# Optimization experiments

Hardware: AMD Instinct MI355X
Metric: run time of the kernel (lower is better)

## Reference

```python
import jax, jax.numpy as jnp
import numpy as np

B, GH, GW, NUM_HEADS, DIM = 8, 32, 32, 16, 1024
HEAD_DIM = DIM // NUM_HEADS  # 64
N = GH * GW  # 1024


def _rope_cos_sin(head_dim, h, w):
    # Lumina-style 2D rotary embedding: head_dim/2 complex rotations,
    # interleaving H-axis and W-axis frequencies: [h0, w0, h1, w1, ...].
    nf = head_dim // 4  # freqs per axis
    theta = 1.0 / (10000.0 ** (np.arange(0, head_dim // 2, 2, dtype=np.float32) / (head_dim // 2)))
    ang_h = np.arange(h, dtype=np.float32)[:, None] * theta[None, :]  # (h, nf)
    ang_w = np.arange(w, dtype=np.float32)[:, None] * theta[None, :]  # (w, nf)
    ang = np.zeros((h, w, head_dim // 2), dtype=np.float32)
    ang[..., 0::2] = ang_h[:, None, :]
    ang[..., 1::2] = ang_w[None, :, :]
    ang = ang.reshape(h * w, head_dim // 2)  # (N, d/2)
    return jnp.asarray(np.cos(ang)), jnp.asarray(np.sin(ang))


def _apply_rope(x, cos, sin):
    # x: (B, nh, N, d); pairs (x[2k], x[2k+1]) form complex numbers,
    # rotated by exp(i*ang) per position. cos/sin: (N, d/2).
    xr, xi = x[..., 0::2], x[..., 1::2]
    out_r = xr * cos - xi * sin
    out_i = xr * sin + xi * cos
    return jnp.stack([out_r, out_i], axis=-1).reshape(x.shape)


def setup_inputs() -> dict:
    key = jax.random.key(0)
    k1, k2, k3 = jax.random.split(key, 3)
    return {
        "x": jax.random.normal(k1, (B, N, DIM), dtype=jnp.float32),
        "wqkv_w": jax.random.normal(k2, (3 * DIM, DIM), dtype=jnp.float32) * 0.02,
        "wqkv_b": jnp.zeros((3 * DIM,), dtype=jnp.float32),
        "out_w": jax.random.normal(k3, (DIM, DIM), dtype=jnp.float32) * 0.02,
        "out_b": jnp.zeros((DIM,), dtype=jnp.float32),
    }


def reference(x, wqkv_w, wqkv_b, out_w, out_b):
    Bs, Ns, C = x.shape
    qkv = x @ wqkv_w.T + wqkv_b  # (B, N, 3*C)
    qkv = qkv.reshape(Bs, Ns, 3, NUM_HEADS, HEAD_DIM).transpose(2, 0, 3, 1, 4)
    q, k, v = qkv[0], qkv[1], qkv[2]  # each (B, nh, N, hd)
    cos, sin = _rope_cos_sin(HEAD_DIM, GH, GW)
    q = _apply_rope(q, cos, sin)
    k = _apply_rope(k, cos, sin)
    scale = HEAD_DIM ** -0.5
    attn = jax.nn.softmax((q * scale) @ jnp.swapaxes(k, -1, -2), axis=-1)  # (B, nh, N, N)
    o = attn @ v  # (B, nh, N, hd)
    o = jnp.swapaxes(o, 1, 2).reshape(Bs, Ns, C)
    out = o @ out_w.T + out_b
    return (out,)
```

## Files before the change

### kernel.cpp

```cpp
#include <hip/hip_runtime.h>
#include <math.h>

#define NB   8
#define NSEQ 1024
#define CDIM 1024
#define NH   16
#define HD   64
#define TC   3072

typedef unsigned short u16;
typedef __attribute__((ext_vector_type(8))) _Float16 f16x8;
typedef __attribute__((ext_vector_type(4))) float f32x4;

#define Q_U   ((size_t)0)
#define K_U   ((size_t)8388608)
#define V_U   ((size_t)16777216)
#define XH_U  ((size_t)25165824)
#define WQH_U ((size_t)33554432)
#define OWH_U ((size_t)36700160)
#define CS_B  ((size_t)100663296)

__device__ inline u16 f16b(float f) {
  union { _Float16 h; u16 u; } c;
  c.h = (_Float16)f;
  return c.u;
}
__device__ inline void gload16(const u16* g, u16* l) {
  __builtin_amdgcn_global_load_lds(
      (const __attribute__((address_space(1))) void*)g,
      (__attribute__((address_space(3))) void*)l, 16, 0, 0);
}

__global__ __launch_bounds__(256) void rope_table_k(float2* __restrict__ cs) {
  int idx = blockIdx.x * 256 + threadIdx.x;
  if (idx >= NSEQ * 32) return;
  int n = idx >> 5, p = idx & 31;
  int t = p >> 1;
  int pos = (p & 1) ? (n & 31) : (n >> 5);
  float th = (float)pow(10000.0, -(double)t / 16.0);
  float ang = (float)pos * th;
  cs[idx] = make_float2(cosf(ang), sinf(ang));
}

__global__ __launch_bounds__(256) void cvtall_k(const float* __restrict__ x,
                                                const float* __restrict__ wq,
                                                const float* __restrict__ ow,
                                                u16* __restrict__ xh,
                                                u16* __restrict__ wqh,
                                                u16* __restrict__ owh) {
  int gi = blockIdx.x * 256 + threadIdx.x;
  const float* src;
  u16* dst;
  int i;
  if (gi < 2097152) {
    src = x; dst = xh; i = gi;
  } else if (gi < 2883584) {
    src = wq; dst = wqh; i = gi - 2097152;
  } else {
    src = ow; dst = owh; i = gi - 2883584;
  }
  float4 v = ((const float4*)src)[i];
  ushort4 h;
  h.x = f16b(v.x); h.y = f16b(v.y); h.z = f16b(v.z); h.w = f16b(v.w);
  ((ushort4*)dst)[i] = h;
}

__global__ __launch_bounds__(512, 1) void qkv8_k(
    const u16* __restrict__ A, const u16* __restrict__ B,
    const float* __restrict__ bias, u16* __restrict__ q,
    u16* __restrict__ k, u16* __restrict__ v, const float2* __restrict__ cs) {
  __shared__ __align__(16) u16 SM[65536];
  const int K = 1024;

  const int bid = blockIdx.y * 8 + blockIdx.x;
  const int swz = (bid & 7) * 64 + (bid >> 3);
  const int bx = swz & 7, by = swz >> 3;
  const int m0 = by * 128, c0 = bx * 384;

  const int t = threadIdx.x;
  const int l = t & 63, w = t >> 6;
  const int wr = w >> 2, wcol = w & 3;
  const int lr = l & 15, lg = l >> 4;

  const int sr = t >> 2;
  const int sgb = (t & 3) ^ ((sr >> 1) & 3);
  const u16* agA = A + (size_t)(m0 + sr) * K + sgb * 8;
  const u16* agB = B + (size_t)(c0 + sr) * K + sgb * 8;
  const size_t rstep = (size_t)128 * K;

  f32x4 acc[4][6] = {};

  auto stage = [&](int kt) {
    u16* base = SM + (kt & 3) * 16384;
    const int ko = kt * 32;
    gload16(agA + ko, base + t * 8);
    gload16(agB + ko, base + 4096 + t * 8);
    gload16(agB + rstep + ko, base + 8192 + t * 8);
    gload16(agB + 2 * rstep + ko, base + 12288 + t * 8);
  };
  auto compute = [&](int kt) {
    const u16* bA = SM + (kt & 3) * 16384;
    const u16* bB = bA + 4096;
    f16x8 bf[6], af[4];
#pragma unroll
    for (int ni = 0; ni < 6; ni++) {
      const int R = wcol * 96 + ni * 16 + lr;
      bf[ni] = *(const f16x8*)(bB + R * 32 + ((lg ^ ((R >> 1) & 3)) * 8));
    }
#pragma unroll
    for (int mi = 0; mi < 4; mi++) {
      const int R = wr * 64 + mi * 16 + lr;
      af[mi] = *(const f16x8*)(bA + R * 32 + ((lg ^ ((R >> 1) & 3)) * 8));
    }
    __builtin_amdgcn_s_setprio(1);
#pragma unroll
    for (int mi = 0; mi < 4; mi++)
#pragma unroll
      for (int ni = 0; ni < 6; ni++)
        acc[mi][ni] =
            __builtin_amdgcn_mfma_f32_16x16x32_f16(af[mi], bf[ni], acc[mi][ni], 0, 0, 0);
    __builtin_amdgcn_s_setprio(0);
  };

  stage(0);
  stage(1);
  stage(2);

  for (int kt = 0; kt < 32; ++kt) {
    if (kt < 30)
      asm volatile("s_waitcnt vmcnt(8)" ::: "memory");
    else if (kt == 30)
      asm volatile("s_waitcnt vmcnt(4)" ::: "memory");
    else
      asm volatile("s_waitcnt vmcnt(0)" ::: "memory");
    __builtin_amdgcn_s_barrier();
    if (kt < 29) stage(kt + 3);
    compute(kt);
  }

#pragma unroll
  for (int ni = 0; ni < 6; ni++) {
    const int cd0 = c0 + wcol * 96 + ni * 16;
    const int which = cd0 >> 10;
    u16* dst = which == 0 ? q : (which == 1 ? k : v);
    const int h = (cd0 & 1023) >> 6;
    const int dbase = cd0 & 63;
    if (which < 2) {
#pragma unroll
      for (int mi = 0; mi < 4; mi++) {
        const int rbase = m0 + wr * 64 + mi * 16 + lg * 4;
        const int d = dbase + lr;
        const float bv = bias[cd0 + lr];
#pragma unroll
        for (int r = 0; r < 4; r++) {
          const int m = rbase + r;
          const int b = m >> 10, n = m & 1023;
          float y = acc[mi][ni][r] + bv;
          float yp = __shfl_xor(y, 1, 64);
          float2 csv = cs[n * 32 + (d >> 1)];
          y = (l & 1) ? fmaf(yp, csv.y, y * csv.x)
                      : fmaf(-yp, csv.y, y * csv.x);
          dst[(((size_t)b * NH + h) * NSEQ + n) * HD + d] = f16b(y);
        }
      }
    } else {
#pragma unroll
      for (int mi = 0; mi < 4; mi++) {
        const int rbase = m0 + wr * 64 + mi * 16 + lg * 4;
        const int b = rbase >> 10, n0r = rbase & 1023;
        const int d = dbase + lr;
        const float bv = bias[cd0 + lr];
        ushort4 pk;
        pk.x = f16b(acc[mi][ni][0] + bv);
        pk.y = f16b(acc[mi][ni][1] + bv);
        pk.z = f16b(acc[mi][ni][2] + bv);
        pk.w = f16b(acc[mi][ni][3] + bv);
        *(ushort4*)&dst[(((size_t)b * NH + h) * HD + d) * NSEQ + n0r] = pk;
      }
    }
  }
}

__global__ __launch_bounds__(512, 1) void mgemm_k(
    const u16* __restrict__ A, const u16* __restrict__ B,
    const float* __restrict__ bias, float* __restrict__ outF, int K) {
  __shared__ __align__(16) u16 SM[49152];

  const int bid = blockIdx.y * 4 + blockIdx.x;
  const int swz = (bid & 7) * 32 + (bid >> 3);
  const int bx = swz & 3, by = swz >> 2;
  const int m0 = by * 128, c0 = bx * 256;

  const int t = threadIdx.x;
  const int l = t & 63, w = t >> 6;
  const int wr = w >> 2, wcol = w & 3;
  const int lr = l & 15, lg = l >> 4;

  const int sr = t >> 2;
  const int sgb = (t & 3) ^ ((sr >> 1) & 3);
  const u16* agA = A + (size_t)(m0 + sr) * K + sgb * 8;
  const u16* agB = B + (size_t)(c0 + sr) * K + sgb * 8;
  const size_t rstep = (size_t)128 * K;

  f32x4 acc[4][4] = {};

  auto stage = [&](int kt) {
    u16* base = SM + (kt & 3) * 12288;
    const int ko = kt * 32;
    gload16(agA + ko, base + t * 8);
    gload16(agB + ko, base + 4096 + t * 8);
    gload16(agB + rstep + ko, base + 8192 + t * 8);
  };
  auto compute = [&](int kt) {
    const u16* bA = SM + (kt & 3) * 12288;
    const u16* bB = bA + 4096;
    f16x8 bf[4], af[4];
#pragma unroll
    for (int ni = 0; ni < 4; ni++) {
      const int R = wcol * 64 + ni * 16 + lr;
      bf[ni] = *(const f16x8*)(bB + R * 32 + ((lg ^ ((R >> 1) & 3)) * 8));
    }
#pragma unroll
    for (int mi = 0; mi < 4; mi++) {
      const int R = wr * 64 + mi * 16 + lr;
      af[mi] = *(const f16x8*)(bA + R * 32 + ((lg ^ ((R >> 1) & 3)) * 8));
    }
    __builtin_amdgcn_s_setprio(1);
#pragma unroll
    for (int mi = 0; mi < 4; mi++)
#pragma unroll
      for (int ni = 0; ni < 4; ni++)
        acc[mi][ni] =
            __builtin_amdgcn_mfma_f32_16x16x32_f16(af[mi], bf[ni], acc[mi][ni], 0, 0, 0);
    __builtin_amdgcn_s_setprio(0);
  };

  stage(0);
  stage(1);
  stage(2);

  for (int kt = 0; kt < 32; ++kt) {
    if (kt < 30)
      asm volatile("s_waitcnt vmcnt(6)" ::: "memory");
    else if (kt == 30)
      asm volatile("s_waitcnt vmcnt(3)" ::: "memory");
    else
      asm volatile("s_waitcnt vmcnt(0)" ::: "memory");
    __builtin_amdgcn_s_barrier();
    if (kt < 29) stage(kt + 3);
    compute(kt);
  }

  float* fl = (float*)SM;
#pragma unroll
  for (int mi = 0; mi < 4; mi++) {
    __syncthreads();
#pragma unroll
    for (int ni = 0; ni < 4; ni++)
#pragma unroll
      for (int r = 0; r < 4; r++)
        fl[(wr * 16 + lg * 4 + r) * 260 + wcol * 64 + ni * 16 + lr] =
            acc[mi][ni][r];
    __syncthreads();
#pragma unroll
    for (int p = 0; p < 4; p++) {
      const int sr2 = (t >> 6) + p * 8;
      const int sc = (t & 63) * 4;
      float4 vv = *(float4*)&fl[sr2 * 260 + sc];
      float4 bv = *(const float4*)&bias[c0 + sc];
      vv.x += bv.x; vv.y += bv.y; vv.z += bv.z; vv.w += bv.w;
      const int grow = m0 + (sr2 >> 4) * 64 + mi * 16 + (sr2 & 15);
      *(float4*)&outF[(size_t)grow * CDIM + c0 + sc] = vv;
    }
  }
}

__global__ __launch_bounds__(256) void attn_k(const u16* __restrict__ qg0,
                                              const u16* __restrict__ kg0,
                                              const u16* __restrict__ vtg0,
                                              u16* __restrict__ og) {
  __shared__ __align__(16) u16 Ks[8192];
  __shared__ __align__(16) u16 Vt[8192];
  __shared__ __align__(16) u16 Ps[4][1024];
  const int t = threadIdx.x;
  const int l = t & 63, w = t >> 6;
  const int lr = l & 15, lg = l >> 4;
  const int bh = blockIdx.x;
  const int n0 = blockIdx.y * 64;

  f16x8 qf[2];
  {
    const u16* qp = qg0 + ((size_t)bh * NSEQ + n0 + w * 16 + lr) * HD + lg * 8;
#pragma unroll
    for (int c = 0; c < 2; c++) {
      f16x8 raw = *(const f16x8*)(qp + c * 32);
#pragma unroll
      for (int j = 0; j < 8; j++) raw[j] = raw[j] * (_Float16)0.125f;
      qf[c] = raw;
    }
  }

  const int r0 = t >> 3, b0 = (t & 7) ^ (r0 & 7);
  const int r1 = (256 + t) >> 3, b1 = ((256 + t) & 7) ^ (r1 & 7);
  const u16* kgb = kg0 + (size_t)bh * NSEQ * HD;
  const u16* vgb = vtg0 + (size_t)bh * HD * NSEQ;
  const u16* kga0 = kgb + r0 * 64 + b0 * 8;
  const u16* kga1 = kgb + r1 * 64 + b1 * 8;
  const u16* vga0 = vgb + r0 * 1024 + b0 * 8;
  const u16* vga1 = vgb + r1 * 1024 + b1 * 8;

  float l_run[4] = {0.f, 0.f, 0.f, 0.f};
  f32x4 oa[4] = {};

  auto stage = [&](int kt) {
    u16* kd = Ks + (kt & 1) * 4096;
    u16* vd = Vt + (kt & 1) * 4096;
    gload16(kga0 + kt * 4096, kd + t * 8);
    gload16(kga1 + kt * 4096, kd + 2048 + t * 8);
    gload16(vga0 + kt * 64, vd + t * 8);
    gload16(vga1 + kt * 64, vd + 2048 + t * 8);
  };

  stage(0);
  for (int kt = 0; kt < 16; kt++) {
    asm volatile("s_waitcnt vmcnt(0)" ::: "memory");
    __builtin_amdgcn_s_barrier();
    if (kt < 15) stage(kt + 1);
    const u16* kb = Ks + (kt & 1) * 4096;
    const u16* vb = Vt + (kt & 1) * 4096;

    f32x4 s[4] = {};
#pragma unroll
    for (int c = 0; c < 2; c++) {
#pragma unroll
      for (int ni = 0; ni < 4; ni++) {
        const int kr = ni * 16 + lr;
        f16x8 kf = *(const f16x8*)&kb[kr * 64 + (((c * 4 + lg) ^ (kr & 7)) * 8)];
        s[ni] = __builtin_amdgcn_mfma_f32_16x16x32_f16(qf[c], kf, s[ni], 0, 0, 0);
      }
    }

#pragma unroll
    for (int r = 0; r < 4; r++) {
      float p[4], ps = 0.f;
#pragma unroll
      for (int ni = 0; ni < 4; ni++) {
        p[ni] = __expf(s[ni][r] - 4.0f);
        ps += p[ni];
      }
      l_run[r] += ps;
      const int prow = lg * 4 + r;
      const int sw = prow & 7;
#pragma unroll
      for (int ni = 0; ni < 4; ni++)
        Ps[w][prow * 64 + (((ni * 2 + (lr >> 3)) ^ sw) * 8) + (lr & 7)] =
            f16b(p[ni]);
    }

#pragma unroll
    for (int c = 0; c < 2; c++) {
      f16x8 pa = *(const f16x8*)&Ps[w][lr * 64 + (((c * 4 + lg) ^ (lr & 7)) * 8)];
#pragma unroll
      for (int ni = 0; ni < 4; ni++) {
        const int dr = ni * 16 + lr;
        f16x8 vf = *(const f16x8*)&vb[dr * 64 + (((c * 4 + lg) ^ (dr & 7)) * 8)];
        oa[ni] = __builtin_amdgcn_mfma_f32_16x16x32_f16(pa, vf, oa[ni], 0, 0, 0);
      }
    }
  }

  const int b = bh >> 4, h = bh & 15;
#pragma unroll
  for (int r = 0; r < 4; r++) {
    float lv = l_run[r];
    lv += __shfl_xor(lv, 1, 64);
    lv += __shfl_xor(lv, 2, 64);
    lv += __shfl_xor(lv, 4, 64);
    lv += __shfl_xor(lv, 8, 64);
    const float inv = 1.0f / lv;
    const size_t n = n0 + w * 16 + lg * 4 + r;
    const size_t base = ((size_t)b * NSEQ + n) * CDIM + h * HD;
#pragma unroll
    for (int ni = 0; ni < 4; ni++)
      og[base + ni * 16 + lr] = f16b(oa[ni][r] * inv);
  }
}

extern "C" void kernel_launch(void* const* d_in, const int* in_sizes, int n_in,
                              void* d_out, int out_size, void* d_ws, size_t ws_size,
                              hipStream_t stream) {
  const float* x      = (const float*)d_in[0];
  const float* wqkv_w = (const float*)d_in[1];
  const float* wqkv_b = (const float*)d_in[2];
  const float* out_w  = (const float*)d_in[3];
  const float* out_b  = (const float*)d_in[4];
  float* out = (float*)d_out;
  u16* ws = (u16*)d_ws;
  float2* cs = (float2*)((char*)d_ws + CS_B);

  rope_table_k<<<dim3((NSEQ * 32 + 255) / 256), 256, 0, stream>>>(cs);
  cvtall_k<<<dim3(12288), 256, 0, stream>>>(
      x, wqkv_w, out_w, ws + XH_U, ws + WQH_U, ws + OWH_U);

  qkv8_k<<<dim3(8, 64), 512, 0, stream>>>(
      ws + XH_U, ws + WQH_U, wqkv_b, ws + Q_U, ws + K_U, ws + V_U, cs);

  attn_k<<<dim3(NB * NH, NSEQ / 64), 256, 0, stream>>>(
      ws + Q_U, ws + K_U, ws + V_U, ws + XH_U);

  mgemm_k<<<dim3(4, 64), 512, 0, stream>>>(
      ws + XH_U, ws + OWH_U, out_b, out, CDIM);
}
```

Before: 202.1 us.

## Replace LDS-pipelined GEMMs with direct global-to-register MFMA loads

Both the QKV projection and output projection GEMMs drop the multi-stage LDS staging pipeline (async global-to-LDS loads, vmcnt waits, barriers) and instead load MFMA fragments directly from global memory into registers each k-step. The QKV kernel also changes its tile from 128x384 to 256x256 with 8x4 accumulators per wave and a 12x32 grid, simplifying the epilogue to one head per wave. This removes barrier and LDS traffic but loses cross-wave data sharing through LDS, relying on L1/L2 for reuse, and exposes global latency without explicit prefetch.

```diff
diff --git a/kernel.cpp b/kernel.cpp
--- a/kernel.cpp
+++ b/kernel.cpp
@@ -69,88 +69,55 @@
     const u16* __restrict__ A, const u16* __restrict__ B,
     const float* __restrict__ bias, u16* __restrict__ q,
     u16* __restrict__ k, u16* __restrict__ v, const float2* __restrict__ cs) {
-  __shared__ __align__(16) u16 SM[65536];
   const int K = 1024;
 
-  const int bid = blockIdx.y * 8 + blockIdx.x;
-  const int swz = (bid & 7) * 64 + (bid >> 3);
-  const int bx = swz & 7, by = swz >> 3;
-  const int m0 = by * 128, c0 = bx * 384;
+  const int bid = blockIdx.y * 12 + blockIdx.x;
+  const int swz = (bid & 7) * 48 + (bid >> 3);
+  const int bx = swz % 12, by = swz / 12;
+  const int m0 = by * 256, c0 = bx * 256;
 
   const int t = threadIdx.x;
   const int l = t & 63, w = t >> 6;
   const int wr = w >> 2, wcol = w & 3;
   const int lr = l & 15, lg = l >> 4;
 
-  const int sr = t >> 2;
-  const int sgb = (t & 3) ^ ((sr >> 1) & 3);
-  const u16* agA = A + (size_t)(m0 + sr) * K + sgb * 8;
-  const u16* agB = B + (size_t)(c0 + sr) * K + sgb * 8;
-  const size_t rstep = (size_t)128 * K;
-
-  f32x4 acc[4][6] = {};
-
-  auto stage = [&](int kt) {
-    u16* base = SM + (kt & 3) * 16384;
-    const int ko = kt * 32;
-    gload16(agA + ko, base + t * 8);
-    gload16(agB + ko, base + 4096 + t * 8);
-    gload16(agB + rstep + ko, base + 8192 + t * 8);
-    gload16(agB + 2 * rstep + ko, base + 12288 + t * 8);
-  };
-  auto compute = [&](int kt) {
-    const u16* bA = SM + (kt & 3) * 16384;
-    const u16* bB = bA + 4096;
-    f16x8 bf[6], af[4];
-#pragma unroll
-    for (int ni = 0; ni < 6; ni++) {
-      const int R = wcol * 96 + ni * 16 + lr;
-      bf[ni] = *(const f16x8*)(bB + R * 32 + ((lg ^ ((R >> 1) & 3)) * 8));
-    }
-#pragma unroll
-    for (int mi = 0; mi < 4; mi++) {
-      const int R = wr * 64 + mi * 16 + lr;
-      af[mi] = *(const f16x8*)(bA + R * 32 + ((lg ^ ((R >> 1) & 3)) * 8));
-    }
-    __builtin_amdgcn_s_setprio(1);
-#pragma unroll
-    for (int mi = 0; mi < 4; mi++)
-#pragma unroll
-      for (int ni = 0; ni < 6; ni++)
+  const u16* pa[8];
+  const u16* pb[4];
+#pragma unroll
+  for (int mi = 0; mi < 8; mi++)
+    pa[mi] = A + (size_t)(m0 + wr * 128 + mi * 16 + lr) * K + lg * 8;
+#pragma unroll
+  for (int ni = 0; ni < 4; ni++)
+    pb[ni] = B + (size_t)(c0 + wcol * 64 + ni * 16 + lr) * K + lg * 8;
+
+  f32x4 acc[8][4] = {};
+
+#pragma unroll 2
+  for (int ko = 0; ko < 1024; ko += 32) {
+    f16x8 af[8], bf[4];
+#pragma unroll
+    for (int ni = 0; ni < 4; ni++) bf[ni] = *(const f16x8*)(pb[ni] + ko);
+#pragma unroll
+    for (int mi = 0; mi < 8; mi++) af[mi] = *(const f16x8*)(pa[mi] + ko);
+#pragma unroll
+    for (int mi = 0; mi < 8; mi++)
+#pragma unroll
+      for (int ni = 0; ni < 4; ni++)
         acc[mi][ni] =
             __builtin_amdgcn_mfma_f32_16x16x32_f16(af[mi], bf[ni], acc[mi][ni], 0, 0, 0);
-    __builtin_amdgcn_s_setprio(0);
-  };
-
-  stage(0);
-  stage(1);
-  stage(2);
-
-  for (int kt = 0; kt < 32; ++kt) {
-    if (kt < 30)
-      asm volatile("s_waitcnt vmcnt(8)" ::: "memory");
-    else if (kt == 30)
-      asm volatile("s_waitcnt vmcnt(4)" ::: "memory");
-    else
-      asm volatile("s_waitcnt vmcnt(0)" ::: "memory");
-    __builtin_amdgcn_s_barrier();
-    if (kt < 29) stage(kt + 3);
-    compute(kt);
-  }
-
-#pragma unroll
-  for (int ni = 0; ni < 6; ni++) {
-    const int cd0 = c0 + wcol * 96 + ni * 16;
-    const int which = cd0 >> 10;
-    u16* dst = which == 0 ? q : (which == 1 ? k : v);
-    const int h = (cd0 & 1023) >> 6;
-    const int dbase = cd0 & 63;
-    if (which < 2) {
-#pragma unroll
-      for (int mi = 0; mi < 4; mi++) {
-        const int rbase = m0 + wr * 64 + mi * 16 + lg * 4;
-        const int d = dbase + lr;
-        const float bv = bias[cd0 + lr];
+  }
+
+  const int which = c0 >> 10;
+  u16* dst = which == 0 ? q : (which == 1 ? k : v);
+  const int h = ((c0 & 1023) + wcol * 64) >> 6;
+  if (which < 2) {
+#pragma unroll
+    for (int mi = 0; mi < 8; mi++) {
+      const int rbase = m0 + wr * 128 + mi * 16 + lg * 4;
+#pragma unroll
+      for (int ni = 0; ni < 4; ni++) {
+        const int d = ni * 16 + lr;
+        const float bv = bias[c0 + wcol * 64 + d];
 #pragma unroll
         for (int r = 0; r < 4; r++) {
           const int m = rbase + r;
@@ -163,13 +130,16 @@
           dst[(((size_t)b * NH + h) * NSEQ + n) * HD + d] = f16b(y);
         }
       }
-    } else {
-#pragma unroll
-      for (int mi = 0; mi < 4; mi++) {
-        const int rbase = m0 + wr * 64 + mi * 16 + lg * 4;
-        const int b = rbase >> 10, n0r = rbase & 1023;
-        const int d = dbase + lr;
-        const float bv = bias[cd0 + lr];
+    }
+  } else {
+#pragma unroll
+    for (int mi = 0; mi < 8; mi++) {
+      const int rbase = m0 + wr * 128 + mi * 16 + lg * 4;
+      const int b = rbase >> 10, n0r = rbase & 1023;
+#pragma unroll
+      for (int ni = 0; ni < 4; ni++) {
+        const int d = ni * 16 + lr;
+        const float bv = bias[c0 + wcol * 64 + d];
         ushort4 pk;
         pk.x = f16b(acc[mi][ni][0] + bv);
         pk.y = f16b(acc[mi][ni][1] + bv);
@@ -184,7 +154,7 @@
 __global__ __launch_bounds__(512, 1) void mgemm_k(
     const u16* __restrict__ A, const u16* __restrict__ B,
     const float* __restrict__ bias, float* __restrict__ outF, int K) {
-  __shared__ __align__(16) u16 SM[49152];
+  __shared__ float fl[32 * 260];
 
   const int bid = blockIdx.y * 4 + blockIdx.x;
   const int swz = (bid & 7) * 32 + (bid >> 3);
@@ -196,62 +166,32 @@
   const int wr = w >> 2, wcol = w & 3;
   const int lr = l & 15, lg = l >> 4;
 
-  const int sr = t >> 2;
-  const int sgb = (t & 3) ^ ((sr >> 1) & 3);
-  const u16* agA = A + (size_t)(m0 + sr) * K + sgb * 8;
-  const u16* agB = B + (size_t)(c0 + sr) * K + sgb * 8;
-  const size_t rstep = (size_t)128 * K;
+  const u16* pa[4];
+  const u16* pb[4];
+#pragma unroll
+  for (int mi = 0; mi < 4; mi++)
+    pa[mi] = A + (size_t)(m0 + wr * 64 + mi * 16 + lr) * K + lg * 8;
+#pragma unroll
+  for (int ni = 0; ni < 4; ni++)
+    pb[ni] = B + (size_t)(c0 + wcol * 64 + ni * 16 + lr) * K + lg * 8;
 
   f32x4 acc[4][4] = {};
 
-  auto stage = [&](int kt) {
-    u16* base = SM + (kt & 3) * 12288;
-    const int ko = kt * 32;
-    gload16(agA + ko, base + t * 8);
-    gload16(agB + ko, base + 4096 + t * 8);
-    gload16(agB + rstep + ko, base + 8192 + t * 8);
-  };
-  auto compute = [&](int kt) {
-    const u16* bA = SM + (kt & 3) * 12288;
-    const u16* bB = bA + 4096;
-    f16x8 bf[4], af[4];
-#pragma unroll
-    for (int ni = 0; ni < 4; ni++) {
-      const int R = wcol * 64 + ni * 16 + lr;
-      bf[ni] = *(const f16x8*)(bB + R * 32 + ((lg ^ ((R >> 1) & 3)) * 8));
-    }
-#pragma unroll
-    for (int mi = 0; mi < 4; mi++) {
-      const int R = wr * 64 + mi * 16 + lr;
-      af[mi] = *(const f16x8*)(bA + R * 32 + ((lg ^ ((R >> 1) & 3)) * 8));
-    }
-    __builtin_amdgcn_s_setprio(1);
+#pragma unroll 2
+  for (int ko = 0; ko < 1024; ko += 32) {
+    f16x8 af[4], bf[4];
+#pragma unroll
+    for (int ni = 0; ni < 4; ni++) bf[ni] = *(const f16x8*)(pb[ni] + ko);
+#pragma unroll
+    for (int mi = 0; mi < 4; mi++) af[mi] = *(const f16x8*)(pa[mi] + ko);
 #pragma unroll
     for (int mi = 0; mi < 4; mi++)
 #pragma unroll
       for (int ni = 0; ni < 4; ni++)
         acc[mi][ni] =
             __builtin_amdgcn_mfma_f32_16x16x32_f16(af[mi], bf[ni], acc[mi][ni], 0, 0, 0);
-    __builtin_amdgcn_s_setprio(0);
-  };
-
-  stage(0);
-  stage(1);
-  stage(2);
-
-  for (int kt = 0; kt < 32; ++kt) {
-    if (kt < 30)
-      asm volatile("s_waitcnt vmcnt(6)" ::: "memory");
-    else if (kt == 30)
-      asm volatile("s_waitcnt vmcnt(3)" ::: "memory");
-    else
-      asm volatile("s_waitcnt vmcnt(0)" ::: "memory");
-    __builtin_amdgcn_s_barrier();
-    if (kt < 29) stage(kt + 3);
-    compute(kt);
-  }
-
-  float* fl = (float*)SM;
+  }
+
 #pragma unroll
   for (int mi = 0; mi < 4; mi++) {
     __syncthreads();
@@ -402,7 +342,7 @@
   cvtall_k<<<dim3(12288), 256, 0, stream>>>(
       x, wqkv_w, out_w, ws + XH_U, ws + WQH_U, ws + OWH_U);
 
-  qkv8_k<<<dim3(8, 64), 512, 0, stream>>>(
+  qkv8_k<<<dim3(12, 32), 512, 0, stream>>>(
       ws + XH_U, ws + WQH_U, wqkv_b, ws + Q_U, ws + K_U, ws + V_U, cs);
 
   attn_k<<<dim3(NB * NH, NSEQ / 64), 256, 0, stream>>>(
```

After: 346.1 us. 1.71x slower.
